# Kernel optimization log

Hardware: AMD Instinct MI355X
Metric: run time of the kernel (lower is better)

## Reference

```python
import jax, jax.numpy as jnp
import numpy as np

D_MODEL = 1024
NHEAD = 16
DIM_HEAD = 64
SCALE = DIM_HEAD ** (-0.5)


def setup_inputs() -> dict:
    key = jax.random.key(0)
    ks = jax.random.split(key, 8)
    B, N = 2, 2048
    inner = NHEAD * DIM_HEAD
    s = 0.02
    return {
        "query": jax.random.normal(ks[0], (B, N, D_MODEL), jnp.float32),
        "key": jax.random.normal(ks[1], (B, N, D_MODEL), jnp.float32),
        "value": jax.random.normal(ks[2], (B, N, D_MODEL), jnp.float32),
        "Wq": jax.random.normal(ks[3], (D_MODEL, inner), jnp.float32) * s,
        "Wk": jax.random.normal(ks[4], (D_MODEL, inner), jnp.float32) * s,
        "Wv": jax.random.normal(ks[5], (D_MODEL, inner), jnp.float32) * s,
        "Wo": jax.random.normal(ks[6], (inner, D_MODEL), jnp.float32) * s,
        "bo": jnp.zeros((D_MODEL,), jnp.float32),
    }


def reference(query, key, value, Wq, Wk, Wv, Wo, bo):
    B, Nq, _ = query.shape
    Nk = key.shape[1]
    # projections (no bias), split heads: [B, N, h, d]
    q = (query @ Wq).reshape(B, Nq, NHEAD, DIM_HEAD)
    k = (key @ Wk).reshape(B, Nk, NHEAD, DIM_HEAD)
    v = (value @ Wv).reshape(B, Nk, NHEAD, DIM_HEAD)
    # scores [B, h, Nq, Nk]
    sim = jnp.einsum('bihd,bjhd->bhij', q, k) * SCALE
    attn = jax.nn.softmax(sim, axis=-1)  # dropout p=0.0 -> identity
    out = jnp.einsum('bhij,bjhd->bihd', attn, v).reshape(B, Nq, NHEAD * DIM_HEAD)
    return out @ Wo + bo
```

## Files before the change

kernel.cpp:

```cpp
#include <hip/hip_runtime.h>
#include <stdint.h>

typedef __attribute__((ext_vector_type(8))) short short8;
typedef __attribute__((ext_vector_type(8))) unsigned short ushort8;
typedef __attribute__((ext_vector_type(4))) unsigned short ushort4v;
typedef __attribute__((ext_vector_type(4))) float float4v;

#define D_MODEL 1024
#define NHEAD 16
#define DIM_HEAD 64
#define BATCH 2
#define SEQ 2048
#define BH (BATCH*NHEAD)
#define MROWS (BATCH*SEQ)
#define MK ((size_t)MROWS * D_MODEL)

__device__ __forceinline__ unsigned short f2bf(float f) {
  union { float f; unsigned u; } v; v.f = f;
  unsigned r = v.u + 0x7fffu + ((v.u >> 16) & 1u);
  return (unsigned short)(r >> 16);
}
__device__ __forceinline__ unsigned short f2bf_fast(float f) {
  union { float f; unsigned u; } v; v.f = f;
  return (unsigned short)((v.u + 0x8000u) >> 16);
}

__device__ __forceinline__ void gld16(const unsigned short* g, unsigned short* l) {
  __builtin_amdgcn_global_load_lds(
      (const __attribute__((address_space(1))) unsigned int*)g,
      (__attribute__((address_space(3))) unsigned int*)l, 16, 0, 0);
}

__global__ __launch_bounds__(256) void wtrans_kernel(const float* __restrict__ W0,
    const float* __restrict__ W1, const float* __restrict__ W2,
    const float* __restrict__ W3, unsigned short* __restrict__ WT) {
  __shared__ float tile[32][33];
  const int z = blockIdx.z;
  const float* W = (z == 0) ? W0 : (z == 1) ? W1 : (z == 2) ? W2 : W3;
  const float scale = (z == 0) ? 0.125f : 1.0f;
  unsigned short* dst = WT + ((size_t)z << 20);
  int bn = blockIdx.x * 32;
  int bk = blockIdx.y * 32;
  int tx = threadIdx.x & 31, ty = threadIdx.x >> 5;
#pragma unroll
  for (int i = 0; i < 4; i++)
    tile[ty + i*8][tx] = W[(size_t)(bk + ty + i*8) * D_MODEL + bn + tx];
  __syncthreads();
#pragma unroll
  for (int i = 0; i < 4; i++)
    dst[(size_t)(bn + ty + i*8) * D_MODEL + bk + tx] = f2bf(tile[tx][ty + i*8] * scale);
}

__global__ __launch_bounds__(256) void cast_kernel(const float* __restrict__ q,
    const float* __restrict__ k, const float* __restrict__ v,
    unsigned short* __restrict__ out) {
  const float* src = (blockIdx.y == 0) ? q : (blockIdx.y == 1) ? k : v;
  unsigned short* dst = out + (size_t)blockIdx.y * MK;
  size_t idx = ((size_t)blockIdx.x * 256 + threadIdx.x) * 8;
  float4v a = *(const float4v*)(src + idx);
  float4v b = *(const float4v*)(src + idx + 4);
  ushort8 o;
  o[0] = f2bf(a[0]); o[1] = f2bf(a[1]); o[2] = f2bf(a[2]); o[3] = f2bf(a[3]);
  o[4] = f2bf(b[0]); o[5] = f2bf(b[1]); o[6] = f2bf(b[2]); o[7] = f2bf(b[3]);
  *(ushort8*)(dst + idx) = o;
}

__global__ __launch_bounds__(256) void vtrans_kernel(const unsigned short* __restrict__ Vb,
                                                     unsigned short* __restrict__ VT) {
  __shared__ unsigned short tile[64][72];
  const int bh = blockIdx.x;
  const int b = bh >> 4, h = bh & 15;
  const int n0 = blockIdx.y * 64;
  const int t = threadIdx.x;
#pragma unroll
  for (int p = 0; p < 2; p++) {
    int g = p*256 + t; int row = g >> 3, c = g & 7;
    *(ushort8*)&tile[row][c*8] =
      *(const ushort8*)(Vb + ((size_t)((b*SEQ + n0 + row)*NHEAD + h))*DIM_HEAD + c*8);
  }
  __syncthreads();
  int d = t >> 2, kc = (t & 3) * 16;
  ushort8 o0, o1;
#pragma unroll
  for (int j = 0; j < 8; j++) { o0[j] = tile[kc + j][d]; o1[j] = tile[kc + 8 + j][d]; }
  unsigned short* dst = VT + ((size_t)(bh*DIM_HEAD + d))*SEQ + n0 + kc;
  *(ushort8*)dst = o0;
  *(ushort8*)(dst + 8) = o1;
}

__global__ __launch_bounds__(256, 3) void proj_kernel(const unsigned short* __restrict__ Xbf,
    const unsigned short* __restrict__ WT0, unsigned short* __restrict__ Y0) {
  __shared__ unsigned short Al[128*64];
  __shared__ unsigned short Bl[128*64];
  const int z = blockIdx.z;
  const unsigned short* A  = Xbf + (size_t)z * MK;
  const unsigned short* BT = WT0 + ((size_t)z << 20);
  unsigned short* Y = Y0 + (size_t)z * MK;
  const int m0 = blockIdx.x * 128, n0 = blockIdx.y * 128;
  const int t = threadIdx.x;
  const int lane = t & 63, w = t >> 6, quad = lane >> 4, lid = lane & 15;
  const int wm = w & 1, wn = w >> 1;
  const int r8 = lane >> 3, c8 = (lane & 7) * 8;

  float4v acc[4][4];
#pragma unroll
  for (int i = 0; i < 4; i++)
#pragma unroll
    for (int j = 0; j < 4; j++) acc[i][j] = (float4v)0.0f;

  for (int k0 = 0; k0 < D_MODEL; k0 += 64) {
#pragma unroll
    for (int p = 0; p < 4; p++) {
      int seg = w*4 + p;
      gld16(A  + (size_t)(m0 + seg*8 + r8) * D_MODEL + k0 + c8, &Al[seg*8*64]);
      gld16(BT + (size_t)(n0 + seg*8 + r8) * D_MODEL + k0 + c8, &Bl[seg*8*64]);
    }
    __syncthreads();
#pragma unroll
    for (int kst = 0; kst < 2; kst++) {
      short8 af[4], bfr[4];
#pragma unroll
      for (int i = 0; i < 4; i++)
        af[i] = *(const short8*)&Al[(wm*64 + i*16 + lid)*64 + kst*32 + quad*8];
#pragma unroll
      for (int j = 0; j < 4; j++)
        bfr[j] = *(const short8*)&Bl[(wn*64 + j*16 + lid)*64 + kst*32 + quad*8];
#pragma unroll
      for (int i = 0; i < 4; i++)
#pragma unroll
        for (int j = 0; j < 4; j++)
          acc[i][j] = __builtin_amdgcn_mfma_f32_16x16x32_bf16(af[i], bfr[j], acc[i][j], 0, 0, 0);
    }
    __syncthreads();
  }
#pragma unroll
  for (int i = 0; i < 4; i++)
#pragma unroll
    for (int j = 0; j < 4; j++)
#pragma unroll
      for (int r = 0; r < 4; r++) {
        int row = m0 + wm*64 + i*16 + quad*4 + r;
        int col = n0 + wn*64 + j*16 + lid;
        Y[(size_t)row * D_MODEL + col] = f2bf_fast(acc[i][j][r]);
      }
}

__global__ __launch_bounds__(256, 3) void outproj_kernel(const unsigned short* __restrict__ A,
    const unsigned short* __restrict__ WT, const float* __restrict__ bias,
    float* __restrict__ out) {
  __shared__ unsigned short Al[64*64];
  __shared__ unsigned short Bl[128*64];
  const int m0 = blockIdx.x * 64, n0 = blockIdx.y * 128;
  const int t = threadIdx.x;
  const int lane = t & 63, w = t >> 6, quad = lane >> 4, lid = lane & 15;
  const int wm = w & 1, wn = w >> 1;
  const int r8 = lane >> 3, c8 = (lane & 7) * 8;

  float4v acc[2][4];
#pragma unroll
  for (int i = 0; i < 2; i++)
#pragma unroll
    for (int j = 0; j < 4; j++) acc[i][j] = (float4v)0.0f;

  for (int k0 = 0; k0 < D_MODEL; k0 += 64) {
#pragma unroll
    for (int p = 0; p < 2; p++) {
      int seg = w*2 + p;
      gld16(A + (size_t)(m0 + seg*8 + r8) * D_MODEL + k0 + c8, &Al[seg*8*64]);
    }
#pragma unroll
    for (int p = 0; p < 4; p++) {
      int seg = w*4 + p;
      gld16(WT + (size_t)(n0 + seg*8 + r8) * D_MODEL + k0 + c8, &Bl[seg*8*64]);
    }
    __syncthreads();
#pragma unroll
    for (int kst = 0; kst < 2; kst++) {
      short8 af[2], bfr[4];
#pragma unroll
      for (int i = 0; i < 2; i++)
        af[i] = *(const short8*)&Al[(wm*32 + i*16 + lid)*64 + kst*32 + quad*8];
#pragma unroll
      for (int j = 0; j < 4; j++)
        bfr[j] = *(const short8*)&Bl[(wn*64 + j*16 + lid)*64 + kst*32 + quad*8];
#pragma unroll
      for (int i = 0; i < 2; i++)
#pragma unroll
        for (int j = 0; j < 4; j++)
          acc[i][j] = __builtin_amdgcn_mfma_f32_16x16x32_bf16(af[i], bfr[j], acc[i][j], 0, 0, 0);
    }
    __syncthreads();
  }
#pragma unroll
  for (int i = 0; i < 2; i++)
#pragma unroll
    for (int j = 0; j < 4; j++)
#pragma unroll
      for (int r = 0; r < 4; r++) {
        int row = m0 + wm*32 + i*16 + quad*4 + r;
        int col = n0 + wn*64 + j*16 + lid;
        out[(size_t)row * D_MODEL + col] = acc[i][j][r] + bias[col];
      }
}

#define QB 128
#define KB 64
#define FSTR 72
#define PSTR 68

__global__ __launch_bounds__(256, 2) void flash_kernel(const unsigned short* __restrict__ Q,
    const unsigned short* __restrict__ K, const unsigned short* __restrict__ VT,
    unsigned short* __restrict__ O) {
  __shared__ unsigned short Ql[QB][FSTR];
  __shared__ unsigned short Kl[KB][FSTR];
  __shared__ unsigned short Vt[DIM_HEAD][FSTR];
  __shared__ unsigned short Pl[4][16][PSTR];

  const int bh = blockIdx.x;
  const int b = bh >> 4, h = bh & 15;
  const int q0 = blockIdx.y * QB;
  const int t = threadIdx.x;
  const int lane = t & 63, w = t >> 6, quad = lane >> 4, lid = lane & 15;
  const int prow = t >> 3, pc = (t & 7) * 8;

  {
#pragma unroll
    for (int p = 0; p < 4; p++) {
      int g = p*256 + t; int row = g >> 3, c = g & 7;
      *(ushort8*)&Ql[row][c*8] =
        *(const ushort8*)(Q + ((size_t)((b*SEQ + q0 + row)*NHEAD + h))*DIM_HEAD + c*8);
    }
  }
  __syncthreads();
  short8 qf[2][2];
#pragma unroll
  for (int st = 0; st < 2; st++)
#pragma unroll
    for (int kst = 0; kst < 2; kst++)
      qf[st][kst] = *(const short8*)&Ql[w*32 + st*16 + lid][kst*32 + quad*8];

  float4v o[2][4];
#pragma unroll
  for (int st = 0; st < 2; st++)
#pragma unroll
    for (int i = 0; i < 4; i++) o[st][i] = (float4v)0.0f;
  float ps[2][4];
#pragma unroll
  for (int st = 0; st < 2; st++)
#pragma unroll
    for (int r = 0; r < 4; r++) ps[st][r] = 0.0f;

  ushort8 kr[2], vr[2];
#pragma unroll
  for (int p = 0; p < 2; p++) {
    int row = p*32 + prow;
    kr[p] = *(const ushort8*)(K + ((size_t)((b*SEQ + row)*NHEAD + h))*DIM_HEAD + pc);
    vr[p] = *(const ushort8*)(VT + ((size_t)(bh*DIM_HEAD + row))*SEQ + pc);
  }

  for (int kb = 0; kb < SEQ; kb += KB) {
#pragma unroll
    for (int p = 0; p < 2; p++) {
      int row = p*32 + prow;
      *(ushort8*)&Kl[row][pc] = kr[p];
      *(ushort8*)&Vt[row][pc] = vr[p];
    }
    __syncthreads();

    if (kb + KB < SEQ) {
      const int kn = kb + KB;
#pragma unroll
      for (int p = 0; p < 2; p++) {
        int row = p*32 + prow;
        kr[p] = *(const ushort8*)(K + ((size_t)((b*SEQ + kn + row)*NHEAD + h))*DIM_HEAD + pc);
        vr[p] = *(const ushort8*)(VT + ((size_t)(bh*DIM_HEAD + row))*SEQ + kn + pc);
      }
    }

    float4v s[2][4];
#pragma unroll
    for (int st = 0; st < 2; st++)
#pragma unroll
      for (int n = 0; n < 4; n++) s[st][n] = (float4v)0.0f;
    __builtin_amdgcn_s_setprio(1);
#pragma unroll
    for (int kst = 0; kst < 2; kst++)
#pragma unroll
      for (int n = 0; n < 4; n++) {
        short8 kf = *(const short8*)&Kl[n*16 + lid][kst*32 + quad*8];
        s[0][n] = __builtin_amdgcn_mfma_f32_16x16x32_bf16(qf[0][kst], kf, s[0][n], 0, 0, 0);
        s[1][n] = __builtin_amdgcn_mfma_f32_16x16x32_bf16(qf[1][kst], kf, s[1][n], 0, 0, 0);
      }
    __builtin_amdgcn_s_setprio(0);

    short8 pf[2][2];
#pragma unroll
    for (int st = 0; st < 2; st++) {
#pragma unroll
      for (int n = 0; n < 4; n++)
#pragma unroll
        for (int r = 0; r < 4; r++) {
          float p = __expf(s[st][n][r]);
          ps[st][r] += p;
          Pl[w][quad*4 + r][n*16 + lid] = f2bf_fast(p);
        }
      pf[st][0] = *(const short8*)&Pl[w][lid][quad*8];
      pf[st][1] = *(const short8*)&Pl[w][lid][32 + quad*8];
    }

    __builtin_amdgcn_s_setprio(1);
#pragma unroll
    for (int kst = 0; kst < 2; kst++)
#pragma unroll
      for (int i = 0; i < 4; i++) {
        short8 vf = *(const short8*)&Vt[i*16 + lid][kst*32 + quad*8];
        o[0][i] = __builtin_amdgcn_mfma_f32_16x16x32_bf16(pf[0][kst], vf, o[0][i], 0, 0, 0);
        o[1][i] = __builtin_amdgcn_mfma_f32_16x16x32_bf16(pf[1][kst], vf, o[1][i], 0, 0, 0);
      }
    __builtin_amdgcn_s_setprio(0);
    __syncthreads();
  }

#pragma unroll
  for (int st = 0; st < 2; st++)
#pragma unroll
    for (int r = 0; r < 4; r++) {
      float v = ps[st][r];
      v += __shfl_xor(v, 1); v += __shfl_xor(v, 2);
      v += __shfl_xor(v, 4); v += __shfl_xor(v, 8);
      ps[st][r] = 1.0f / v;
    }
#pragma unroll
  for (int st = 0; st < 2; st++)
#pragma unroll
    for (int i = 0; i < 4; i++)
#pragma unroll
      for (int r = 0; r < 4; r++) {
        int q = q0 + w*32 + st*16 + quad*4 + r;
        O[((size_t)((b*SEQ + q)*NHEAD + h))*DIM_HEAD + i*16 + lid] =
          f2bf(o[st][i][r] * ps[st][r]);
      }
}

extern "C" void kernel_launch(void* const* d_in, const int* in_sizes, int n_in,
                              void* d_out, int out_size, void* d_ws, size_t ws_size,
                              hipStream_t stream) {
  const float* query = (const float*)d_in[0];
  const float* key_  = (const float*)d_in[1];
  const float* value = (const float*)d_in[2];
  const float* Wq = (const float*)d_in[3];
  const float* Wk = (const float*)d_in[4];
  const float* Wv = (const float*)d_in[5];
  const float* Wo = (const float*)d_in[6];
  const float* bo = (const float*)d_in[7];
  float* out = (float*)d_out;

  char* ws = (char*)d_ws;
  unsigned short* WqT = (unsigned short*)(ws + (0ll  << 20));
  unsigned short* WoT = (unsigned short*)(ws + (6ll  << 20));
  unsigned short* Xbf = (unsigned short*)(ws + (8ll  << 20));
  unsigned short* Qb  = (unsigned short*)(ws + (32ll << 20));
  unsigned short* Kb  = Qb + MK;
  unsigned short* Vb  = Qb + 2*MK;
  unsigned short* VT  = (unsigned short*)(ws + (8ll  << 20));
  unsigned short* Ob  = (unsigned short*)(ws + (16ll << 20));

  dim3 tb(256);
  dim3 tg(32, 32, 4);
  hipLaunchKernelGGL(wtrans_kernel, tg, tb, 0, stream, Wq, Wk, Wv, Wo, WqT);

  dim3 cg(MK / (256*8), 3);
  hipLaunchKernelGGL(cast_kernel, cg, tb, 0, stream, query, key_, value, Xbf);

  dim3 pg(MROWS/128, D_MODEL/128, 3);
  hipLaunchKernelGGL(proj_kernel, pg, tb, 0, stream, Xbf, WqT, Qb);

  dim3 vg(BH, SEQ/64);
  hipLaunchKernelGGL(vtrans_kernel, vg, tb, 0, stream, Vb, VT);

  dim3 fg(BH, SEQ/QB);
  hipLaunchKernelGGL(flash_kernel, fg, tb, 0, stream, Qb, Kb, VT, Ob);

  dim3 og(MROWS/64, D_MODEL/128);
  hipLaunchKernelGGL(outproj_kernel, og, tb, 0, stream, Ob, WoT, bo, out);
}
```

Before: 227.5 us.

## Split flash attention across 8 waves of 16 rows with permuted V layout

```diff
diff --git a/kernel.cpp b/kernel.cpp
--- a/kernel.cpp
+++ b/kernel.cpp
@@ -79,11 +79,15 @@
       *(const ushort8*)(Vb + ((size_t)((b*SEQ + n0 + row)*NHEAD + h))*DIM_HEAD + c*8);
   }
   __syncthreads();
-  int d = t >> 2, kc = (t & 3) * 16;
+  int d = t >> 2, base = (t & 3) * 16, b2 = (t & 3) * 4;
   ushort8 o0, o1;
 #pragma unroll
-  for (int j = 0; j < 8; j++) { o0[j] = tile[kc + j][d]; o1[j] = tile[kc + 8 + j][d]; }
-  unsigned short* dst = VT + ((size_t)(bh*DIM_HEAD + d))*SEQ + n0 + kc;
+  for (int m = 0; m < 8; m++) {
+    int k0_ = (m & 3)*16 + b2 + (m >> 2);
+    o0[m] = tile[k0_][d];
+    o1[m] = tile[k0_ + 2][d];
+  }
+  unsigned short* dst = VT + ((size_t)(bh*DIM_HEAD + d))*SEQ + n0 + base;
   *(ushort8*)dst = o0;
   *(ushort8*)(dst + 8) = o1;
 }
@@ -206,15 +210,13 @@
 #define QB 128
 #define KB 64
 #define FSTR 72
-#define PSTR 68
-
-__global__ __launch_bounds__(256, 2) void flash_kernel(const unsigned short* __restrict__ Q,
+
+__global__ __launch_bounds__(512, 2) void flash_kernel(const unsigned short* __restrict__ Q,
     const unsigned short* __restrict__ K, const unsigned short* __restrict__ VT,
     unsigned short* __restrict__ O) {
-  __shared__ unsigned short Ql[QB][FSTR];
   __shared__ unsigned short Kl[KB][FSTR];
   __shared__ unsigned short Vt[DIM_HEAD][FSTR];
-  __shared__ unsigned short Pl[4][16][PSTR];
+  __shared__ unsigned short Pl[8][16][FSTR];
 
   const int bh = blockIdx.x;
   const int b = bh >> 4, h = bh & 15;
@@ -223,90 +225,60 @@
   const int lane = t & 63, w = t >> 6, quad = lane >> 4, lid = lane & 15;
   const int prow = t >> 3, pc = (t & 7) * 8;
 
-  {
-#pragma unroll
-    for (int p = 0; p < 4; p++) {
-      int g = p*256 + t; int row = g >> 3, c = g & 7;
-      *(ushort8*)&Ql[row][c*8] =
-        *(const ushort8*)(Q + ((size_t)((b*SEQ + q0 + row)*NHEAD + h))*DIM_HEAD + c*8);
-    }
-  }
-  __syncthreads();
-  short8 qf[2][2];
-#pragma unroll
-  for (int st = 0; st < 2; st++)
-#pragma unroll
-    for (int kst = 0; kst < 2; kst++)
-      qf[st][kst] = *(const short8*)&Ql[w*32 + st*16 + lid][kst*32 + quad*8];
-
-  float4v o[2][4];
-#pragma unroll
-  for (int st = 0; st < 2; st++)
-#pragma unroll
-    for (int i = 0; i < 4; i++) o[st][i] = (float4v)0.0f;
-  float ps[2][4];
-#pragma unroll
-  for (int st = 0; st < 2; st++)
-#pragma unroll
-    for (int r = 0; r < 4; r++) ps[st][r] = 0.0f;
-
-  ushort8 kr[2], vr[2];
-#pragma unroll
-  for (int p = 0; p < 2; p++) {
-    int row = p*32 + prow;
-    kr[p] = *(const ushort8*)(K + ((size_t)((b*SEQ + row)*NHEAD + h))*DIM_HEAD + pc);
-    vr[p] = *(const ushort8*)(VT + ((size_t)(bh*DIM_HEAD + row))*SEQ + pc);
-  }
+  short8 qf[2];
+#pragma unroll
+  for (int kst = 0; kst < 2; kst++)
+    qf[kst] = *(const short8*)(Q +
+        ((size_t)((b*SEQ + q0 + w*16 + lid)*NHEAD + h))*DIM_HEAD + kst*32 + quad*8);
+
+  float4v o[4];
+#pragma unroll
+  for (int i = 0; i < 4; i++) o[i] = (float4v)0.0f;
+  float ps[4];
+#pragma unroll
+  for (int r = 0; r < 4; r++) ps[r] = 0.0f;
+
+  ushort8 kr = *(const ushort8*)(K + ((size_t)((b*SEQ + prow)*NHEAD + h))*DIM_HEAD + pc);
+  ushort8 vr = *(const ushort8*)(VT + ((size_t)(bh*DIM_HEAD + prow))*SEQ + pc);
 
   for (int kb = 0; kb < SEQ; kb += KB) {
-#pragma unroll
-    for (int p = 0; p < 2; p++) {
-      int row = p*32 + prow;
-      *(ushort8*)&Kl[row][pc] = kr[p];
-      *(ushort8*)&Vt[row][pc] = vr[p];
-    }
+    *(ushort8*)&Kl[prow][pc] = kr;
+    *(ushort8*)&Vt[prow][pc] = vr;
     __syncthreads();
 
     if (kb + KB < SEQ) {
       const int kn = kb + KB;
-#pragma unroll
-      for (int p = 0; p < 2; p++) {
-        int row = p*32 + prow;
-        kr[p] = *(const ushort8*)(K + ((size_t)((b*SEQ + kn + row)*NHEAD + h))*DIM_HEAD + pc);
-        vr[p] = *(const ushort8*)(VT + ((size_t)(bh*DIM_HEAD + row))*SEQ + kn + pc);
-      }
-    }
-
-    float4v s[2][4];
-#pragma unroll
-    for (int st = 0; st < 2; st++)
-#pragma unroll
-      for (int n = 0; n < 4; n++) s[st][n] = (float4v)0.0f;
+      kr = *(const ushort8*)(K + ((size_t)((b*SEQ + kn + prow)*NHEAD + h))*DIM_HEAD + pc);
+      vr = *(const ushort8*)(VT + ((size_t)(bh*DIM_HEAD + prow))*SEQ + kn + pc);
+    }
+
+    float4v s[4];
+#pragma unroll
+    for (int n = 0; n < 4; n++) s[n] = (float4v)0.0f;
     __builtin_amdgcn_s_setprio(1);
 #pragma unroll
     for (int kst = 0; kst < 2; kst++)
 #pragma unroll
       for (int n = 0; n < 4; n++) {
         short8 kf = *(const short8*)&Kl[n*16 + lid][kst*32 + quad*8];
-        s[0][n] = __builtin_amdgcn_mfma_f32_16x16x32_bf16(qf[0][kst], kf, s[0][n], 0, 0, 0);
-        s[1][n] = __builtin_amdgcn_mfma_f32_16x16x32_bf16(qf[1][kst], kf, s[1][n], 0, 0, 0);
+        s[n] = __builtin_amdgcn_mfma_f32_16x16x32_bf16(qf[kst], kf, s[n], 0, 0, 0);
       }
     __builtin_amdgcn_s_setprio(0);
 
-    short8 pf[2][2];
-#pragma unroll
-    for (int st = 0; st < 2; st++) {
-#pragma unroll
-      for (int n = 0; n < 4; n++)
-#pragma unroll
-        for (int r = 0; r < 4; r++) {
-          float p = __expf(s[st][n][r]);
-          ps[st][r] += p;
-          Pl[w][quad*4 + r][n*16 + lid] = f2bf_fast(p);
-        }
-      pf[st][0] = *(const short8*)&Pl[w][lid][quad*8];
-      pf[st][1] = *(const short8*)&Pl[w][lid][32 + quad*8];
-    }
+#pragma unroll
+    for (int r = 0; r < 4; r++) {
+      ushort4v pk;
+#pragma unroll
+      for (int n = 0; n < 4; n++) {
+        float p = __expf(s[n][r]);
+        ps[r] += p;
+        pk[n] = f2bf_fast(p);
+      }
+      *(ushort4v*)&Pl[w][quad*4 + r][lid*4] = pk;
+    }
+    short8 pf[2];
+    pf[0] = *(const short8*)&Pl[w][lid][quad*8];
+    pf[1] = *(const short8*)&Pl[w][lid][32 + quad*8];
 
     __builtin_amdgcn_s_setprio(1);
 #pragma unroll
@@ -314,32 +286,27 @@
 #pragma unroll
       for (int i = 0; i < 4; i++) {
         short8 vf = *(const short8*)&Vt[i*16 + lid][kst*32 + quad*8];
-        o[0][i] = __builtin_amdgcn_mfma_f32_16x16x32_bf16(pf[0][kst], vf, o[0][i], 0, 0, 0);
-        o[1][i] = __builtin_amdgcn_mfma_f32_16x16x32_bf16(pf[1][kst], vf, o[1][i], 0, 0, 0);
+        o[i] = __builtin_amdgcn_mfma_f32_16x16x32_bf16(pf[kst], vf, o[i], 0, 0, 0);
       }
     __builtin_amdgcn_s_setprio(0);
     __syncthreads();
   }
 
 #pragma unroll
-  for (int st = 0; st < 2; st++)
+  for (int r = 0; r < 4; r++) {
+    float v = ps[r];
+    v += __shfl_xor(v, 1); v += __shfl_xor(v, 2);
+    v += __shfl_xor(v, 4); v += __shfl_xor(v, 8);
+    ps[r] = 1.0f / v;
+  }
+#pragma unroll
+  for (int i = 0; i < 4; i++)
 #pragma unroll
     for (int r = 0; r < 4; r++) {
-      float v = ps[st][r];
-      v += __shfl_xor(v, 1); v += __shfl_xor(v, 2);
-      v += __shfl_xor(v, 4); v += __shfl_xor(v, 8);
-      ps[st][r] = 1.0f / v;
-    }
-#pragma unroll
-  for (int st = 0; st < 2; st++)
-#pragma unroll
-    for (int i = 0; i < 4; i++)
-#pragma unroll
-      for (int r = 0; r < 4; r++) {
-        int q = q0 + w*32 + st*16 + quad*4 + r;
-        O[((size_t)((b*SEQ + q)*NHEAD + h))*DIM_HEAD + i*16 + lid] =
-          f2bf(o[st][i][r] * ps[st][r]);
-      }
+      int q = q0 + w*16 + quad*4 + r;
+      O[((size_t)((b*SEQ + q)*NHEAD + h))*DIM_HEAD + i*16 + lid] =
+        f2bf(o[i][r] * ps[r]);
+    }
 }
 
 extern "C" void kernel_launch(void* const* d_in, const int* in_sizes, int n_in,
@@ -378,8 +345,9 @@
   dim3 vg(BH, SEQ/64);
   hipLaunchKernelGGL(vtrans_kernel, vg, tb, 0, stream, Vb, VT);
 
+  dim3 tb2(512);
   dim3 fg(BH, SEQ/QB);
-  hipLaunchKernelGGL(flash_kernel, fg, tb, 0, stream, Qb, Kb, VT, Ob);
+  hipLaunchKernelGGL(flash_kernel, fg, tb2, 0, stream, Qb, Kb, VT, Ob);
 
   dim3 og(MROWS/64, D_MODEL/128);
   hipLaunchKernelGGL(outproj_kernel, og, tb, 0, stream, Ob, WoT, bo, out);
```

After: 225.3 us. No clear change (-1.0%).

## Compute transposed scores in registers and double-buffer K/V tiles in flash kernel

Applied to the files above, without the earlier changes.

```diff
diff --git a/kernel.cpp b/kernel.cpp
--- a/kernel.cpp
+++ b/kernel.cpp
@@ -79,11 +79,17 @@
       *(const ushort8*)(Vb + ((size_t)((b*SEQ + n0 + row)*NHEAD + h))*DIM_HEAD + c*8);
   }
   __syncthreads();
-  int d = t >> 2, kc = (t & 3) * 16;
+  int d = t >> 2, base = (t & 3) * 16;
   ushort8 o0, o1;
 #pragma unroll
-  for (int j = 0; j < 8; j++) { o0[j] = tile[kc + j][d]; o1[j] = tile[kc + 8 + j][d]; }
-  unsigned short* dst = VT + ((size_t)(bh*DIM_HEAD + d))*SEQ + n0 + kc;
+  for (int m = 0; m < 8; m++) {
+    int e0 = base + m, e1 = base + 8 + m;
+    int k0_ = 32*(e0>>5) + 16*((e0>>2)&1) + 4*((e0>>3)&3) + (e0&3);
+    int k1_ = 32*(e1>>5) + 16*((e1>>2)&1) + 4*((e1>>3)&3) + (e1&3);
+    o0[m] = tile[k0_][d];
+    o1[m] = tile[k1_][d];
+  }
+  unsigned short* dst = VT + ((size_t)(bh*DIM_HEAD + d))*SEQ + n0 + base;
   *(ushort8*)dst = o0;
   *(ushort8*)(dst + 8) = o1;
 }
@@ -206,15 +212,13 @@
 #define QB 128
 #define KB 64
 #define FSTR 72
-#define PSTR 68
+#define NT (SEQ/KB)
 
 __global__ __launch_bounds__(256, 2) void flash_kernel(const unsigned short* __restrict__ Q,
     const unsigned short* __restrict__ K, const unsigned short* __restrict__ VT,
     unsigned short* __restrict__ O) {
-  __shared__ unsigned short Ql[QB][FSTR];
-  __shared__ unsigned short Kl[KB][FSTR];
-  __shared__ unsigned short Vt[DIM_HEAD][FSTR];
-  __shared__ unsigned short Pl[4][16][PSTR];
+  __shared__ unsigned short Kl[2][KB][FSTR];
+  __shared__ unsigned short Vt[2][DIM_HEAD][FSTR];
 
   const int bh = blockIdx.x;
   const int b = bh >> 4, h = bh & 15;
@@ -223,60 +227,41 @@
   const int lane = t & 63, w = t >> 6, quad = lane >> 4, lid = lane & 15;
   const int prow = t >> 3, pc = (t & 7) * 8;
 
-  {
-#pragma unroll
-    for (int p = 0; p < 4; p++) {
-      int g = p*256 + t; int row = g >> 3, c = g & 7;
-      *(ushort8*)&Ql[row][c*8] =
-        *(const ushort8*)(Q + ((size_t)((b*SEQ + q0 + row)*NHEAD + h))*DIM_HEAD + c*8);
-    }
-  }
-  __syncthreads();
+  const unsigned short* Kbase = K + ((size_t)(b*SEQ)*NHEAD + h)*DIM_HEAD;
+  const unsigned short* Vbase = VT + (size_t)bh*DIM_HEAD*SEQ;
+
   short8 qf[2][2];
 #pragma unroll
   for (int st = 0; st < 2; st++)
 #pragma unroll
     for (int kst = 0; kst < 2; kst++)
-      qf[st][kst] = *(const short8*)&Ql[w*32 + st*16 + lid][kst*32 + quad*8];
+      qf[st][kst] = *(const short8*)(Q +
+          ((size_t)((b*SEQ + q0 + w*32 + st*16 + lid)*NHEAD + h))*DIM_HEAD + kst*32 + quad*8);
 
   float4v o[2][4];
 #pragma unroll
   for (int st = 0; st < 2; st++)
 #pragma unroll
     for (int i = 0; i < 4; i++) o[st][i] = (float4v)0.0f;
-  float ps[2][4];
-#pragma unroll
-  for (int st = 0; st < 2; st++)
-#pragma unroll
-    for (int r = 0; r < 4; r++) ps[st][r] = 0.0f;
-
-  ushort8 kr[2], vr[2];
-#pragma unroll
-  for (int p = 0; p < 2; p++) {
-    int row = p*32 + prow;
-    kr[p] = *(const ushort8*)(K + ((size_t)((b*SEQ + row)*NHEAD + h))*DIM_HEAD + pc);
-    vr[p] = *(const ushort8*)(VT + ((size_t)(bh*DIM_HEAD + row))*SEQ + pc);
-  }
-
-  for (int kb = 0; kb < SEQ; kb += KB) {
+  float ps[2] = {0.0f, 0.0f};
+
+  auto LOADT = [&](int kb, ushort8* kr, ushort8* vr) {
 #pragma unroll
     for (int p = 0; p < 2; p++) {
       int row = p*32 + prow;
-      *(ushort8*)&Kl[row][pc] = kr[p];
-      *(ushort8*)&Vt[row][pc] = vr[p];
-    }
-    __syncthreads();
-
-    if (kb + KB < SEQ) {
-      const int kn = kb + KB;
-#pragma unroll
-      for (int p = 0; p < 2; p++) {
-        int row = p*32 + prow;
-        kr[p] = *(const ushort8*)(K + ((size_t)((b*SEQ + kn + row)*NHEAD + h))*DIM_HEAD + pc);
-        vr[p] = *(const ushort8*)(VT + ((size_t)(bh*DIM_HEAD + row))*SEQ + kn + pc);
-      }
-    }
-
+      kr[p] = *(const ushort8*)(Kbase + (size_t)(kb + row) * D_MODEL + pc);
+      vr[p] = *(const ushort8*)(Vbase + (size_t)row * SEQ + kb + pc);
+    }
+  };
+  auto COMMIT = [&](int bi, const ushort8* kr, const ushort8* vr) {
+#pragma unroll
+    for (int p = 0; p < 2; p++) {
+      int row = p*32 + prow;
+      *(ushort8*)&Kl[bi][row][pc] = kr[p];
+      *(ushort8*)&Vt[bi][row][pc] = vr[p];
+    }
+  };
+  auto STEP = [&](int bi) {
     float4v s[2][4];
 #pragma unroll
     for (int st = 0; st < 2; st++)
@@ -287,49 +272,61 @@
     for (int kst = 0; kst < 2; kst++)
 #pragma unroll
       for (int n = 0; n < 4; n++) {
-        short8 kf = *(const short8*)&Kl[n*16 + lid][kst*32 + quad*8];
-        s[0][n] = __builtin_amdgcn_mfma_f32_16x16x32_bf16(qf[0][kst], kf, s[0][n], 0, 0, 0);
-        s[1][n] = __builtin_amdgcn_mfma_f32_16x16x32_bf16(qf[1][kst], kf, s[1][n], 0, 0, 0);
+        short8 kf = *(const short8*)&Kl[bi][n*16 + lid][kst*32 + quad*8];
+        s[0][n] = __builtin_amdgcn_mfma_f32_16x16x32_bf16(kf, qf[0][kst], s[0][n], 0, 0, 0);
+        s[1][n] = __builtin_amdgcn_mfma_f32_16x16x32_bf16(kf, qf[1][kst], s[1][n], 0, 0, 0);
       }
     __builtin_amdgcn_s_setprio(0);
-
-    short8 pf[2][2];
-#pragma unroll
-    for (int st = 0; st < 2; st++) {
-#pragma unroll
-      for (int n = 0; n < 4; n++)
-#pragma unroll
-        for (int r = 0; r < 4; r++) {
-          float p = __expf(s[st][n][r]);
-          ps[st][r] += p;
-          Pl[w][quad*4 + r][n*16 + lid] = f2bf_fast(p);
-        }
-      pf[st][0] = *(const short8*)&Pl[w][lid][quad*8];
-      pf[st][1] = *(const short8*)&Pl[w][lid][32 + quad*8];
-    }
-
+    short8 pf0[2], pf1[2];
+#pragma unroll
+    for (int n = 0; n < 4; n++)
+#pragma unroll
+      for (int r = 0; r < 4; r++) {
+        float p0 = __expf(s[0][n][r]);
+        float p1 = __expf(s[1][n][r]);
+        ps[0] += p0; ps[1] += p1;
+        pf0[n >> 1][4*(n & 1) + r] = (short)f2bf_fast(p0);
+        pf1[n >> 1][4*(n & 1) + r] = (short)f2bf_fast(p1);
+      }
     __builtin_amdgcn_s_setprio(1);
 #pragma unroll
     for (int kst = 0; kst < 2; kst++)
 #pragma unroll
       for (int i = 0; i < 4; i++) {
-        short8 vf = *(const short8*)&Vt[i*16 + lid][kst*32 + quad*8];
-        o[0][i] = __builtin_amdgcn_mfma_f32_16x16x32_bf16(pf[0][kst], vf, o[0][i], 0, 0, 0);
-        o[1][i] = __builtin_amdgcn_mfma_f32_16x16x32_bf16(pf[1][kst], vf, o[1][i], 0, 0, 0);
+        short8 vf = *(const short8*)&Vt[bi][i*16 + lid][kst*32 + quad*8];
+        o[0][i] = __builtin_amdgcn_mfma_f32_16x16x32_bf16(pf0[kst], vf, o[0][i], 0, 0, 0);
+        o[1][i] = __builtin_amdgcn_mfma_f32_16x16x32_bf16(pf1[kst], vf, o[1][i], 0, 0, 0);
       }
     __builtin_amdgcn_s_setprio(0);
-    __syncthreads();
-  }
-
-#pragma unroll
-  for (int st = 0; st < 2; st++)
-#pragma unroll
-    for (int r = 0; r < 4; r++) {
-      float v = ps[st][r];
-      v += __shfl_xor(v, 1); v += __shfl_xor(v, 2);
-      v += __shfl_xor(v, 4); v += __shfl_xor(v, 8);
-      ps[st][r] = 1.0f / v;
-    }
+  };
+
+  ushort8 krA[2], vrA[2], krB[2], vrB[2];
+  LOADT(0, krA, vrA);
+  LOADT(KB, krB, vrB);
+  COMMIT(0, krA, vrA);
+  __syncthreads();
+
+  for (int i = 0; i < NT; i += 2) {
+    if (i + 2 < NT) LOADT((i + 2)*KB, krA, vrA);
+    STEP(0);
+    if (i + 1 < NT) COMMIT(1, krB, vrB);
+    __syncthreads();
+    if (i + 3 < NT) LOADT((i + 3)*KB, krB, vrB);
+    STEP(1);
+    if (i + 2 < NT) COMMIT(0, krA, vrA);
+    __syncthreads();
+  }
+
+  float dr[2][4];
+#pragma unroll
+  for (int st = 0; st < 2; st++) {
+    float v = ps[st];
+    v += __shfl_xor(v, 16);
+    v += __shfl_xor(v, 32);
+    v = 1.0f / v;
+#pragma unroll
+    for (int r = 0; r < 4; r++) dr[st][r] = __shfl(v, quad*4 + r);
+  }
 #pragma unroll
   for (int st = 0; st < 2; st++)
 #pragma unroll
@@ -338,7 +335,7 @@
       for (int r = 0; r < 4; r++) {
         int q = q0 + w*32 + st*16 + quad*4 + r;
         O[((size_t)((b*SEQ + q)*NHEAD + h))*DIM_HEAD + i*16 + lid] =
-          f2bf(o[st][i][r] * ps[st][r]);
+          f2bf(o[st][i][r] * dr[st][r]);
       }
 }
 
```

After: 214.4 us. 5.8% less time.
